# Kernel optimization log

Measured on AMD Instinct MI355X. Metric: run time of the kernel, lower is better.

Reference implementation:

```python
import math
import jax, jax.numpy as jnp
import numpy as np


def _proj(x, w, b):
    # 1x1x1 Conv3d == pointwise channel matmul: (B,C,T,H,W) x (O,C) -> (B,O,T,H,W)
    return jnp.einsum('bcthw,oc->bothw', x, w) + b[None, :, None, None, None]


def setup_inputs() -> dict:
    key = jax.random.key(0)
    ks = jax.random.split(key, 16)
    B, C, T, H, W = 2, 64, 16, 14, 14
    CI = C // 2
    s_in = 1.0 / math.sqrt(C)
    s_out = 1.0 / math.sqrt(CI)
    inp = {'x': jax.random.normal(ks[0], (B, C, T, H, W), jnp.float32)}
    # QKV projections for spatial (s) and temporal (t) branches: (CI, C) weights
    pnames = ['qs', 'ks', 'vs', 'qt', 'kt', 'vt']
    for i, n in enumerate(pnames):
        inp['W' + n] = jax.random.normal(ks[1 + i], (CI, C), jnp.float32) * s_in
        inp['b' + n] = jax.random.normal(ks[7 + i], (CI,), jnp.float32) * 0.01
    # output projection W: (C, CI)
    inp['Ww'] = jax.random.normal(ks[13], (C, CI), jnp.float32) * s_out
    inp['bw'] = jax.random.normal(ks[14], (C,), jnp.float32) * 0.01
    return inp


def reference(x, Wqs, bqs, Wks, bks, Wvs, bvs, Wqt, bqt, Wkt, bkt, Wvt, bvt, Ww, bw):
    B, C, T, H, W = x.shape
    CI = Wqs.shape[0]
    N = CI * H * W  # flat dim after original's raw .view (mixes channel & spatial/time)
    scale = 1.0 / math.sqrt(T)

    # ---- spatial branch: .view(B, T, -1) raw reshape of (B,CI,T,H,W) ----
    qs = _proj(x, Wqs, bqs).reshape(B, T, N).transpose(0, 2, 1)   # (B,N,T)
    ks_ = _proj(x, Wks, bks).reshape(B, T, N)                     # (B,T,N)
    vs = _proj(x, Wvs, bvs).reshape(B, T, N).transpose(0, 2, 1)   # (B,N,T)
    attn_s = jax.nn.softmax(jnp.einsum('bnt,btm->bnm', qs, ks_) * scale, axis=-1)  # (B,N,N)
    ys = jnp.einsum('bnm,bmt->bnt', attn_s, vs)                   # (B,N,T)
    ys = ys.transpose(0, 2, 1).reshape(B, CI, T, H, W)

    # ---- temporal branch: .view(B, CI*H*W, -1) raw reshape ----
    qt = _proj(x, Wqt, bqt).reshape(B, N, T).transpose(0, 2, 1)   # (B,T,N)
    kt = _proj(x, Wkt, bkt).reshape(B, N, T)                      # (B,N,T)
    vt = _proj(x, Wvt, bvt).reshape(B, N, T).transpose(0, 2, 1)   # (B,T,N)
    attn_t = jax.nn.softmax(jnp.einsum('btn,bns->bts', qt, kt) * scale, axis=-1)  # (B,T,T)
    yt = jnp.einsum('bts,bsn->btn', attn_t, vt)                   # (B,T,N)
    yt = yt.transpose(0, 2, 1).reshape(B, CI, T, H, W)

    y = ys + yt
    return _proj(y, Ww, bw) + x
```

## Files before the change

### kernel.cpp

```cpp
#include <hip/hip_runtime.h>
#include <math.h>

#define S3   3136
#define PB   100352
#define XB   200704
#define NN   6272
#define MW   7
#define MPW  896
#define TGC  49

typedef __attribute__((ext_vector_type(8))) short bf16x8;
typedef __attribute__((ext_vector_type(4))) float f32x4;
typedef __attribute__((ext_vector_type(16))) float f32x16;
typedef __attribute__((ext_vector_type(4))) uint u32x4;

__device__ inline ushort f2bf(float f) {
    uint u = __float_as_uint(f);
    return (ushort)((u + 0x7FFFu + ((u >> 16) & 1u)) >> 16);
}

__device__ inline uint cvtpk(float lo, float hi) {
    uint r;
    asm("v_cvt_pk_bf16_f32 %0, %1, %2" : "=v"(r) : "v"(lo), "v"(hi));
    return r;
}

__device__ inline void swap32(uint &a, uint &b) {
    asm("v_permlane32_swap_b32 %0, %1" : "+v"(a), "+v"(b));
}

__global__ __launch_bounds__(256) void proj_kernel(
    const float* __restrict__ x,
    const float* __restrict__ W0, const float* __restrict__ b0,
    const float* __restrict__ W1, const float* __restrict__ b1,
    const float* __restrict__ W2, const float* __restrict__ b2,
    const float* __restrict__ W3, const float* __restrict__ b3,
    const float* __restrict__ W4, const float* __restrict__ b4,
    const float* __restrict__ W5, const float* __restrict__ b5,
    ushort* __restrict__ Qb, ushort* __restrict__ Kb, ushort* __restrict__ Vb,
    float* __restrict__ Qt, float* __restrict__ Kt, float* __restrict__ Vt)
{
    const float* Wp; const float* bp;
    switch (blockIdx.y) {
        case 0:  Wp = W0; bp = b0; break;
        case 1:  Wp = W1; bp = b1; break;
        case 2:  Wp = W2; bp = b2; break;
        case 3:  Wp = W3; bp = b3; break;
        case 4:  Wp = W4; bp = b4; break;
        default: Wp = W5; bp = b5; break;
    }
    int z = blockIdx.z;

    int gid = blockIdx.x * 256 + threadIdx.x;
    if (gid >= 2 * S3) return;
    int b = (gid >= S3) ? 1 : 0;
    int s = gid - b * S3;

    float xr[64];
    #pragma unroll
    for (int c = 0; c < 64; ++c) xr[c] = x[(size_t)b * XB + (size_t)c * S3 + s];

    float a[16];
    #pragma unroll
    for (int oo = 0; oo < 16; ++oo) {
        int o = z * 16 + oo;
        float acc = bp[o];
        #pragma unroll
        for (int c = 0; c < 64; ++c) acc = fmaf(Wp[o * 64 + c], xr[c], acc);
        a[oo] = acc;
    }

    if (blockIdx.y < 2) {
        const float sc = (blockIdx.y == 0) ? 0.36067376022224085f : 1.0f;
        ushort* ob = (blockIdx.y == 0) ? Qb : Kb;
        #pragma unroll
        for (int h = 0; h < 2; ++h) {
            int n = h * S3 + s;
            uint u0 = f2bf(a[0 + h] * sc)  | ((uint)f2bf(a[2 + h]  * sc) << 16);
            uint u1 = f2bf(a[4 + h] * sc)  | ((uint)f2bf(a[6 + h]  * sc) << 16);
            uint u2 = f2bf(a[8 + h] * sc)  | ((uint)f2bf(a[10 + h] * sc) << 16);
            uint u3 = f2bf(a[12 + h] * sc) | ((uint)f2bf(a[14 + h] * sc) << 16);
            *(uint4*)(ob + ((size_t)(b * NN + n) * 16 + z * 8)) = make_uint4(u0, u1, u2, u3);
        }
    } else if (blockIdx.y == 2) {
        #pragma unroll
        for (int oo = 0; oo < 16; ++oo) {
            int o = z * 16 + oo;
            Vb[(size_t)(b * 16 + (o >> 1)) * NN + (o & 1) * S3 + s] = f2bf(a[oo]);
        }
    } else {
        float* op = (blockIdx.y == 3) ? Qt : (blockIdx.y == 4) ? Kt : Vt;
        #pragma unroll
        for (int oo = 0; oo < 16; ++oo)
            op[(size_t)b * PB + (size_t)(z * 16 + oo) * S3 + s] = a[oo];
    }
}

__global__ __launch_bounds__(256) void attn_kernel(
    const ushort* __restrict__ Qb, const ushort* __restrict__ Kb,
    const ushort* __restrict__ Vb, const float* __restrict__ Qt,
    const float* __restrict__ Kt,
    float* __restrict__ Pacc, float* __restrict__ Pl, float* __restrict__ Gp)
{
    __shared__ float qs[128 * 16], ks[128 * 16];

    int b = blockIdx.y;

    if (blockIdx.x >= 343) {
        int c = blockIdx.x - 343;
        size_t base = (size_t)b * PB + (size_t)c * 2048;
        for (int i = threadIdx.x; i < 512; i += 256) {
            ((float4*)qs)[i] = ((const float4*)(Qt + base))[i];
            ((float4*)ks)[i] = ((const float4*)(Kt + base))[i];
        }
        __syncthreads();
        int t = threadIdx.x >> 4, s = threadIdx.x & 15;
        float acc = 0.0f;
        #pragma unroll 8
        for (int n = 0; n < 128; ++n)
            acc = fmaf(qs[n * 16 + t], ks[n * 16 + s], acc);
        Gp[(size_t)(b * TGC + c) * 256 + threadIdx.x] = acc;
        return;
    }

    int wave = __builtin_amdgcn_readfirstlane((int)(threadIdx.x >> 6));
    int lane = threadIdx.x & 63;
    int col  = lane & 31;
    int h    = lane >> 5;
    int gw   = blockIdx.x * 4 + wave;
    int ntile = gw / 7;
    int w     = gw - ntile * 7;
    int nbase = ntile * 32;
    int m0    = w * MPW;

    bf16x8 qf = *(const bf16x8*)(Qb + ((size_t)(b * NN + nbase + col) * 16 + h * 8));

    const bf16x8 vzero = {0, 0, 0, 0, 0, 0, 0, 0};
    const bf16x8 vones = {16256, 16256, 16256, 16256, 16256, 16256, 16256, 16256};
    f32x16 yacc;
    #pragma unroll
    for (int r = 0; r < 16; ++r) yacc[r] = 0.0f;
    f32x16 zero16 = yacc;

    #pragma unroll 2
    for (int it = 0; it < MPW / 32; ++it) {
        int mb = m0 + it * 32;
        bf16x8 kf = *(const bf16x8*)(Kb + ((size_t)(b * NN + mb + col) * 16 + h * 8));
        bf16x8 vf0 = vzero, vf1 = vzero;
        if (col < 16) {
            const ushort* vp = Vb + ((size_t)(b * 16 + col) * NN + mb + h * 8);
            vf0 = *(const bf16x8*)(vp);
            vf1 = *(const bf16x8*)(vp + 16);
        } else if (col == 16) { vf0 = vones; vf1 = vones; }

        f32x16 st = __builtin_amdgcn_mfma_f32_32x32x16_bf16(kf, qf, zero16, 0, 0, 0);
        float pv[16];
        #pragma unroll
        for (int r = 0; r < 16; ++r) pv[r] = __builtin_amdgcn_exp2f(st[r]);

        uint X0 = cvtpk(pv[0],  pv[1]),  X1 = cvtpk(pv[2],  pv[3]);
        uint Y0 = cvtpk(pv[4],  pv[5]),  Y1 = cvtpk(pv[6],  pv[7]);
        uint X2 = cvtpk(pv[8],  pv[9]),  X3 = cvtpk(pv[10], pv[11]);
        uint Y2 = cvtpk(pv[12], pv[13]), Y3 = cvtpk(pv[14], pv[15]);
        swap32(X0, Y0); swap32(X1, Y1);
        swap32(X2, Y2); swap32(X3, Y3);
        u32x4 pb0 = {X0, X1, Y0, Y1};
        u32x4 pb1 = {X2, X3, Y2, Y3};

        yacc = __builtin_amdgcn_mfma_f32_32x32x16_bf16(
                   vf0, __builtin_bit_cast(bf16x8, pb0), yacc, 0, 0, 0);
        yacc = __builtin_amdgcn_mfma_f32_32x32x16_bf16(
                   vf1, __builtin_bit_cast(bf16x8, pb1), yacc, 0, 0, 0);
    }

    #pragma unroll
    for (int r = 0; r < 8; ++r) {
        int t = (r & 3) + 8 * (r >> 2) + 4 * h;
        Pacc[((size_t)(b * 16 + t) * MW + w) * NN + nbase + col] = yacc[r];
    }
    if (h == 0)
        Pl[((size_t)b * MW + w) * NN + nbase + col] = yacc[8];
}

__global__ __launch_bounds__(256) void merge_final(
    const float* __restrict__ Pacc, const float* __restrict__ Pl,
    const float* __restrict__ Gp, const float* __restrict__ Vt,
    const float* __restrict__ x, const float* __restrict__ Ww,
    const float* __restrict__ bw, float* __restrict__ out)
{
    __shared__ float Lsh[256];
    __shared__ float Ash[16][17];
    __shared__ float Wsh[64 * 36];
    __shared__ float Ysh[16 * 36];

    int b  = blockIdx.y;
    int sc = blockIdx.x;

    {
        float a = 0.0f;
        for (int c = 0; c < TGC; ++c)
            a += Gp[(size_t)(b * TGC + c) * 256 + threadIdx.x];
        Lsh[threadIdx.x] = a * 0.25f;
        for (int i = threadIdx.x; i < 2048; i += 256)
            Wsh[(i >> 5) * 36 + (i & 31)] = Ww[i];
    }
    __syncthreads();
    if (threadIdx.x < 16) {
        int t = threadIdx.x;
        const float* Lr = &Lsh[t * 16];
        float mx = -1e30f;
        #pragma unroll
        for (int s = 0; s < 16; ++s) mx = fmaxf(mx, Lr[s]);
        float e[16]; float sm = 0.0f;
        #pragma unroll
        for (int s = 0; s < 16; ++s) { e[s] = __expf(Lr[s] - mx); sm += e[s]; }
        float inv = 1.0f / sm;
        #pragma unroll
        for (int s = 0; s < 16; ++s) Ash[s][t] = e[s] * inv;
    }
    __syncthreads();

    #pragma unroll
    for (int k = 0; k < 2; ++k) {
        int idx = threadIdx.x + k * 256;
        int ss = idx & 15;
        int ci = idx >> 4;
        int s  = sc * 16 + ss;
        int t  = ci >> 1;
        int nn = (ci & 1) * S3 + s;

        float a = 0.0f, l = 0.0f;
        #pragma unroll
        for (int w = 0; w < MW; ++w) {
            a += Pacc[((size_t)(b * 16 + t) * MW + w) * NN + nn];
            l += Pl[((size_t)b * MW + w) * NN + nn];
        }
        float ys = a / l;

        int t2 = nn & 15;
        const float4* vp = (const float4*)(Vt + (size_t)b * PB + (size_t)t * NN + (nn & ~15));
        float4 v0 = vp[0], v1 = vp[1], v2 = vp[2], v3 = vp[3];
        float yt = Ash[0][t2] * v0.x;
        yt = fmaf(Ash[1][t2],  v0.y, yt); yt = fmaf(Ash[2][t2],  v0.z, yt);
        yt = fmaf(Ash[3][t2],  v0.w, yt); yt = fmaf(Ash[4][t2],  v1.x, yt);
        yt = fmaf(Ash[5][t2],  v1.y, yt); yt = fmaf(Ash[6][t2],  v1.z, yt);
        yt = fmaf(Ash[7][t2],  v1.w, yt); yt = fmaf(Ash[8][t2],  v2.x, yt);
        yt = fmaf(Ash[9][t2],  v2.y, yt); yt = fmaf(Ash[10][t2], v2.z, yt);
        yt = fmaf(Ash[11][t2], v2.w, yt); yt = fmaf(Ash[12][t2], v3.x, yt);
        yt = fmaf(Ash[13][t2], v3.y, yt); yt = fmaf(Ash[14][t2], v3.z, yt);
        yt = fmaf(Ash[15][t2], v3.w, yt);

        Ysh[ss * 36 + ci] = ys + yt;
    }
    __syncthreads();

    int ss = threadIdx.x & 15;
    int cg = threadIdx.x >> 4;
    int s  = sc * 16 + ss;

    float acc[4];
    #pragma unroll
    for (int k = 0; k < 4; ++k) acc[k] = bw[cg * 4 + k];

    #pragma unroll
    for (int cb = 0; cb < 32; cb += 4) {
        float4 y4 = *(const float4*)&Ysh[ss * 36 + cb];
        #pragma unroll
        for (int k = 0; k < 4; ++k) {
            float4 w4 = *(const float4*)&Wsh[(cg * 4 + k) * 36 + cb];
            acc[k] = fmaf(w4.x, y4.x, acc[k]);
            acc[k] = fmaf(w4.y, y4.y, acc[k]);
            acc[k] = fmaf(w4.z, y4.z, acc[k]);
            acc[k] = fmaf(w4.w, y4.w, acc[k]);
        }
    }

    #pragma unroll
    for (int k = 0; k < 4; ++k) {
        int c = cg * 4 + k;
        size_t o = (size_t)b * XB + (size_t)c * S3 + s;
        out[o] = x[o] + acc[k];
    }
}

extern "C" void kernel_launch(void* const* d_in, const int* in_sizes, int n_in,
                              void* d_out, int out_size, void* d_ws, size_t ws_size,
                              hipStream_t stream)
{
    const float* x   = (const float*)d_in[0];
    const float* Wqs = (const float*)d_in[1];  const float* bqs = (const float*)d_in[2];
    const float* Wks = (const float*)d_in[3];  const float* bks = (const float*)d_in[4];
    const float* Wvs = (const float*)d_in[5];  const float* bvs = (const float*)d_in[6];
    const float* Wqt = (const float*)d_in[7];  const float* bqt = (const float*)d_in[8];
    const float* Wkt = (const float*)d_in[9];  const float* bkt = (const float*)d_in[10];
    const float* Wvt = (const float*)d_in[11]; const float* bvt = (const float*)d_in[12];
    const float* Ww  = (const float*)d_in[13]; const float* bw  = (const float*)d_in[14];

    float* ws = (float*)d_ws;
    ushort* Qb = (ushort*)(ws);
    ushort* Kb = (ushort*)(ws + 100352);
    ushort* Vb = (ushort*)(ws + 200704);
    float* Qt  = ws + 301056;
    float* Kt  = ws + 501760;
    float* Vt  = ws + 702464;
    float* Gp  = ws + 903168;
    float* Pacc = ws + 928256;
    float* Pl   = ws + 2333184;

    proj_kernel<<<dim3(25, 6, 2), 256, 0, stream>>>(
        x, Wqs, bqs, Wks, bks, Wvs, bvs, Wqt, bqt, Wkt, bkt, Wvt, bvt,
        Qb, Kb, Vb, Qt, Kt, Vt);

    attn_kernel<<<dim3(343 + TGC, 2), 256, 0, stream>>>(
        Qb, Kb, Vb, Qt, Kt, Pacc, Pl, Gp);

    merge_final<<<dim3(196, 2), 256, 0, stream>>>(
        Pacc, Pl, Gp, Vt, x, Ww, bw, (float*)d_out);
}
```

Before: 131.0 us.

## Fuse three kernels into one persistent kernel with software grid barriers

```diff
diff --git a/kernel.cpp b/kernel.cpp
--- a/kernel.cpp
+++ b/kernel.cpp
@@ -10,7 +10,6 @@
 #define TGC  49
 
 typedef __attribute__((ext_vector_type(8))) short bf16x8;
-typedef __attribute__((ext_vector_type(4))) float f32x4;
 typedef __attribute__((ext_vector_type(16))) float f32x16;
 typedef __attribute__((ext_vector_type(4))) uint u32x4;
 
@@ -29,7 +28,27 @@
     asm("v_permlane32_swap_b32 %0, %1" : "+v"(a), "+v"(b));
 }
 
-__global__ __launch_bounds__(256) void proj_kernel(
+__device__ inline void gridbar(uint* bar, int phase) {
+    __syncthreads();
+    if (threadIdx.x == 0) {
+        uint* grp  = bar + phase * 528 + ((blockIdx.x >> 4) << 4);
+        uint* root = bar + phase * 528 + 512;
+        uint old = __hip_atomic_fetch_add(grp, 1u, __ATOMIC_ACQ_REL,
+                                          __HIP_MEMORY_SCOPE_AGENT);
+        if (old == 15u)
+            __hip_atomic_fetch_add(root, 1u, __ATOMIC_ACQ_REL,
+                                   __HIP_MEMORY_SCOPE_AGENT);
+        long spins = 0;
+        while (__hip_atomic_load(root, __ATOMIC_ACQUIRE,
+                                 __HIP_MEMORY_SCOPE_AGENT) < 32u) {
+            __builtin_amdgcn_s_sleep(8);
+            if (++spins > 20000000L) break;
+        }
+    }
+    __syncthreads();
+}
+
+__global__ __launch_bounds__(256, 2) void fused_kernel(
     const float* __restrict__ x,
     const float* __restrict__ W0, const float* __restrict__ b0,
     const float* __restrict__ W1, const float* __restrict__ b1,
@@ -37,249 +56,254 @@
     const float* __restrict__ W3, const float* __restrict__ b3,
     const float* __restrict__ W4, const float* __restrict__ b4,
     const float* __restrict__ W5, const float* __restrict__ b5,
+    const float* __restrict__ Ww, const float* __restrict__ bw,
     ushort* __restrict__ Qb, ushort* __restrict__ Kb, ushort* __restrict__ Vb,
-    float* __restrict__ Qt, float* __restrict__ Kt, float* __restrict__ Vt)
+    float* __restrict__ Qt, float* __restrict__ Kt, float* __restrict__ Vt,
+    float* __restrict__ Gp, float* __restrict__ Pacc, float* __restrict__ Pl,
+    uint* __restrict__ bar, float* __restrict__ out)
 {
-    const float* Wp; const float* bp;
-    switch (blockIdx.y) {
-        case 0:  Wp = W0; bp = b0; break;
-        case 1:  Wp = W1; bp = b1; break;
-        case 2:  Wp = W2; bp = b2; break;
-        case 3:  Wp = W3; bp = b3; break;
-        case 4:  Wp = W4; bp = b4; break;
-        default: Wp = W5; bp = b5; break;
+    __shared__ float shpool[4096];
+    int bid = blockIdx.x;
+    int tid = threadIdx.x;
+
+    if (bid < 300) {
+        int u  = bid;
+        int bx = u % 25;
+        int yq = (u / 25) % 6;
+        int z  = u / 150;
+        const float* Wp; const float* bp;
+        switch (yq) {
+            case 0:  Wp = W0; bp = b0; break;
+            case 1:  Wp = W1; bp = b1; break;
+            case 2:  Wp = W2; bp = b2; break;
+            case 3:  Wp = W3; bp = b3; break;
+            case 4:  Wp = W4; bp = b4; break;
+            default: Wp = W5; bp = b5; break;
+        }
+        int gid = bx * 256 + tid;
+        if (gid < 2 * S3) {
+            int b = (gid >= S3) ? 1 : 0;
+            int s = gid - b * S3;
+
+            float xr[64];
+            #pragma unroll
+            for (int c = 0; c < 64; ++c) xr[c] = x[(size_t)b * XB + (size_t)c * S3 + s];
+
+            float a[16];
+            #pragma unroll
+            for (int oo = 0; oo < 16; ++oo) {
+                int o = z * 16 + oo;
+                float acc = bp[o];
+                #pragma unroll
+                for (int c = 0; c < 64; ++c) acc = fmaf(Wp[o * 64 + c], xr[c], acc);
+                a[oo] = acc;
+            }
+
+            if (yq < 2) {
+                const float sc = (yq == 0) ? 0.36067376022224085f : 1.0f;
+                ushort* ob = (yq == 0) ? Qb : Kb;
+                #pragma unroll
+                for (int h = 0; h < 2; ++h) {
+                    int n = h * S3 + s;
+                    uint u0 = f2bf(a[0 + h] * sc)  | ((uint)f2bf(a[2 + h]  * sc) << 16);
+                    uint u1 = f2bf(a[4 + h] * sc)  | ((uint)f2bf(a[6 + h]  * sc) << 16);
+                    uint u2 = f2bf(a[8 + h] * sc)  | ((uint)f2bf(a[10 + h] * sc) << 16);
+                    uint u3 = f2bf(a[12 + h] * sc) | ((uint)f2bf(a[14 + h] * sc) << 16);
+                    *(uint4*)(ob + ((size_t)(b * NN + n) * 16 + z * 8)) = make_uint4(u0, u1, u2, u3);
+                }
+            } else if (yq == 2) {
+                #pragma unroll
+                for (int oo = 0; oo < 16; ++oo) {
+                    int o = z * 16 + oo;
+                    Vb[(size_t)(b * 16 + (o >> 1)) * NN + (o & 1) * S3 + s] = f2bf(a[oo]);
+                }
+            } else {
+                float* op = (yq == 3) ? Qt : (yq == 4) ? Kt : Vt;
+                #pragma unroll
+                for (int oo = 0; oo < 16; ++oo)
+                    op[(size_t)b * PB + (size_t)(z * 16 + oo) * S3 + s] = a[oo];
+            }
+        }
     }
-    int z = blockIdx.z;
-
-    int gid = blockIdx.x * 256 + threadIdx.x;
-    if (gid >= 2 * S3) return;
-    int b = (gid >= S3) ? 1 : 0;
-    int s = gid - b * S3;
-
-    float xr[64];
-    #pragma unroll
-    for (int c = 0; c < 64; ++c) xr[c] = x[(size_t)b * XB + (size_t)c * S3 + s];
-
-    float a[16];
-    #pragma unroll
-    for (int oo = 0; oo < 16; ++oo) {
-        int o = z * 16 + oo;
-        float acc = bp[o];
+    gridbar(bar, 0);
+
+    for (int u = bid; u < 784; u += 512) {
+        int xb = u % 392;
+        int b  = u / 392;
+
+        if (xb >= 343) {
+            int c = xb - 343;
+            float* qs = shpool;
+            float* ks = shpool + 2048;
+            size_t base = (size_t)b * PB + (size_t)c * 2048;
+            for (int i = tid; i < 512; i += 256) {
+                ((float4*)qs)[i] = ((const float4*)(Qt + base))[i];
+                ((float4*)ks)[i] = ((const float4*)(Kt + base))[i];
+            }
+            __syncthreads();
+            int t = tid >> 4, s = tid & 15;
+            float acc = 0.0f;
+            #pragma unroll 8
+            for (int n = 0; n < 128; ++n)
+                acc = fmaf(qs[n * 16 + t], ks[n * 16 + s], acc);
+            Gp[(size_t)(b * TGC + c) * 256 + tid] = acc;
+            __syncthreads();
+        } else {
+            int wave = __builtin_amdgcn_readfirstlane(tid >> 6);
+            int lane = tid & 63;
+            int col  = lane & 31;
+            int h    = lane >> 5;
+            int gw   = xb * 4 + wave;
+            int ntile = gw / 7;
+            int w     = gw - ntile * 7;
+            int nbase = ntile * 32;
+            int m0    = w * MPW;
+
+            bf16x8 qf = *(const bf16x8*)(Qb + ((size_t)(b * NN + nbase + col) * 16 + h * 8));
+
+            const bf16x8 vzero = {0, 0, 0, 0, 0, 0, 0, 0};
+            const bf16x8 vones = {16256, 16256, 16256, 16256, 16256, 16256, 16256, 16256};
+            f32x16 yacc;
+            #pragma unroll
+            for (int r = 0; r < 16; ++r) yacc[r] = 0.0f;
+            f32x16 zero16 = yacc;
+
+            #pragma unroll 2
+            for (int it = 0; it < MPW / 32; ++it) {
+                int mb = m0 + it * 32;
+                bf16x8 kf = *(const bf16x8*)(Kb + ((size_t)(b * NN + mb + col) * 16 + h * 8));
+                bf16x8 vf0 = vzero, vf1 = vzero;
+                if (col < 16) {
+                    const ushort* vp = Vb + ((size_t)(b * 16 + col) * NN + mb + h * 8);
+                    vf0 = *(const bf16x8*)(vp);
+                    vf1 = *(const bf16x8*)(vp + 16);
+                } else if (col == 16) { vf0 = vones; vf1 = vones; }
+
+                f32x16 st = __builtin_amdgcn_mfma_f32_32x32x16_bf16(kf, qf, zero16, 0, 0, 0);
+                float pv[16];
+                #pragma unroll
+                for (int r = 0; r < 16; ++r) pv[r] = __builtin_amdgcn_exp2f(st[r]);
+
+                uint X0 = cvtpk(pv[0],  pv[1]),  X1 = cvtpk(pv[2],  pv[3]);
+                uint Y0 = cvtpk(pv[4],  pv[5]),  Y1 = cvtpk(pv[6],  pv[7]);
+                uint X2 = cvtpk(pv[8],  pv[9]),  X3 = cvtpk(pv[10], pv[11]);
+                uint Y2 = cvtpk(pv[12], pv[13]), Y3 = cvtpk(pv[14], pv[15]);
+                swap32(X0, Y0); swap32(X1, Y1);
+                swap32(X2, Y2); swap32(X3, Y3);
+                u32x4 pb0 = {X0, X1, Y0, Y1};
+                u32x4 pb1 = {X2, X3, Y2, Y3};
+
+                yacc = __builtin_amdgcn_mfma_f32_32x32x16_bf16(
+                           vf0, __builtin_bit_cast(bf16x8, pb0), yacc, 0, 0, 0);
+                yacc = __builtin_amdgcn_mfma_f32_32x32x16_bf16(
+                           vf1, __builtin_bit_cast(bf16x8, pb1), yacc, 0, 0, 0);
+            }
+
+            #pragma unroll
+            for (int r = 0; r < 8; ++r) {
+                int t = (r & 3) + 8 * (r >> 2) + 4 * h;
+                Pacc[((size_t)(b * 16 + t) * MW + w) * NN + nbase + col] = yacc[r];
+            }
+            if (h == 0)
+                Pl[((size_t)b * MW + w) * NN + nbase + col] = yacc[8];
+        }
+    }
+    gridbar(bar, 1);
+
+    if (bid < 392) {
+        int b  = bid / 196;
+        int sc = bid % 196;
+
+        float* Lsh  = shpool;
+        float* AshF = shpool + 256;
+        float* Wsh  = shpool + 544;
+        float* Ysh  = shpool + 2848;
+
+        {
+            float a = 0.0f;
+            for (int c = 0; c < TGC; ++c)
+                a += Gp[(size_t)(b * TGC + c) * 256 + tid];
+            Lsh[tid] = a * 0.25f;
+            for (int i = tid; i < 2048; i += 256)
+                Wsh[(i >> 5) * 36 + (i & 31)] = Ww[i];
+        }
+        __syncthreads();
+        if (tid < 16) {
+            int t = tid;
+            const float* Lr = &Lsh[t * 16];
+            float mx = -1e30f;
+            #pragma unroll
+            for (int s = 0; s < 16; ++s) mx = fmaxf(mx, Lr[s]);
+            float e[16]; float sm = 0.0f;
+            #pragma unroll
+            for (int s = 0; s < 16; ++s) { e[s] = __expf(Lr[s] - mx); sm += e[s]; }
+            float inv = 1.0f / sm;
+            #pragma unroll
+            for (int s = 0; s < 16; ++s) AshF[s * 17 + t] = e[s] * inv;
+        }
+        __syncthreads();
+
         #pragma unroll
-        for (int c = 0; c < 64; ++c) acc = fmaf(Wp[o * 64 + c], xr[c], acc);
-        a[oo] = acc;
-    }
-
-    if (blockIdx.y < 2) {
-        const float sc = (blockIdx.y == 0) ? 0.36067376022224085f : 1.0f;
-        ushort* ob = (blockIdx.y == 0) ? Qb : Kb;
+        for (int k = 0; k < 2; ++k) {
+            int idx = tid + k * 256;
+            int ss = idx & 15;
+            int ci = idx >> 4;
+            int s  = sc * 16 + ss;
+            int t  = ci >> 1;
+            int nn = (ci & 1) * S3 + s;
+
+            float a = 0.0f, l = 0.0f;
+            #pragma unroll
+            for (int w = 0; w < MW; ++w) {
+                a += Pacc[((size_t)(b * 16 + t) * MW + w) * NN + nn];
+                l += Pl[((size_t)b * MW + w) * NN + nn];
+            }
+            float ys = a / l;
+
+            int t2 = nn & 15;
+            const float4* vp = (const float4*)(Vt + (size_t)b * PB + (size_t)t * NN + (nn & ~15));
+            float4 v0 = vp[0], v1 = vp[1], v2 = vp[2], v3 = vp[3];
+            float yt = AshF[0 * 17 + t2] * v0.x;
+            yt = fmaf(AshF[1 * 17 + t2],  v0.y, yt); yt = fmaf(AshF[2 * 17 + t2],  v0.z, yt);
+            yt = fmaf(AshF[3 * 17 + t2],  v0.w, yt); yt = fmaf(AshF[4 * 17 + t2],  v1.x, yt);
+            yt = fmaf(AshF[5 * 17 + t2],  v1.y, yt); yt = fmaf(AshF[6 * 17 + t2],  v1.z, yt);
+            yt = fmaf(AshF[7 * 17 + t2],  v1.w, yt); yt = fmaf(AshF[8 * 17 + t2],  v2.x, yt);
+            yt = fmaf(AshF[9 * 17 + t2],  v2.y, yt); yt = fmaf(AshF[10 * 17 + t2], v2.z, yt);
+            yt = fmaf(AshF[11 * 17 + t2], v2.w, yt); yt = fmaf(AshF[12 * 17 + t2], v3.x, yt);
+            yt = fmaf(AshF[13 * 17 + t2], v3.y, yt); yt = fmaf(AshF[14 * 17 + t2], v3.z, yt);
+            yt = fmaf(AshF[15 * 17 + t2], v3.w, yt);
+
+            Ysh[ss * 36 + ci] = ys + yt;
+        }
+        __syncthreads();
+
+        int ss = tid & 15;
+        int cg2 = tid >> 4;
+        int s  = sc * 16 + ss;
+
+        float acc[4];
         #pragma unroll
-        for (int h = 0; h < 2; ++h) {
-            int n = h * S3 + s;
-            uint u0 = f2bf(a[0 + h] * sc)  | ((uint)f2bf(a[2 + h]  * sc) << 16);
-            uint u1 = f2bf(a[4 + h] * sc)  | ((uint)f2bf(a[6 + h]  * sc) << 16);
-            uint u2 = f2bf(a[8 + h] * sc)  | ((uint)f2bf(a[10 + h] * sc) << 16);
-            uint u3 = f2bf(a[12 + h] * sc) | ((uint)f2bf(a[14 + h] * sc) << 16);
-            *(uint4*)(ob + ((size_t)(b * NN + n) * 16 + z * 8)) = make_uint4(u0, u1, u2, u3);
-        }
-    } else if (blockIdx.y == 2) {
+        for (int k = 0; k < 4; ++k) acc[k] = bw[cg2 * 4 + k];
+
         #pragma unroll
-        for (int oo = 0; oo < 16; ++oo) {
-            int o = z * 16 + oo;
-            Vb[(size_t)(b * 16 + (o >> 1)) * NN + (o & 1) * S3 + s] = f2bf(a[oo]);
-        }
-    } else {
-        float* op = (blockIdx.y == 3) ? Qt : (blockIdx.y == 4) ? Kt : Vt;
-        #pragma unroll
-        for (int oo = 0; oo < 16; ++oo)
-            op[(size_t)b * PB + (size_t)(z * 16 + oo) * S3 + s] = a[oo];
-    }
-}
-
-__global__ __launch_bounds__(256) void attn_kernel(
-    const ushort* __restrict__ Qb, const ushort* __restrict__ Kb,
-    const ushort* __restrict__ Vb, const float* __restrict__ Qt,
-    const float* __restrict__ Kt,
-    float* __restrict__ Pacc, float* __restrict__ Pl, float* __restrict__ Gp)
-{
-    __shared__ float qs[128 * 16], ks[128 * 16];
-
-    int b = blockIdx.y;
-
-    if (blockIdx.x >= 343) {
-        int c = blockIdx.x - 343;
-        size_t base = (size_t)b * PB + (size_t)c * 2048;
-        for (int i = threadIdx.x; i < 512; i += 256) {
-            ((float4*)qs)[i] = ((const float4*)(Qt + base))[i];
-            ((float4*)ks)[i] = ((const float4*)(Kt + base))[i];
-        }
-        __syncthreads();
-        int t = threadIdx.x >> 4, s = threadIdx.x & 15;
-        float acc = 0.0f;
-        #pragma unroll 8
-        for (int n = 0; n < 128; ++n)
-            acc = fmaf(qs[n * 16 + t], ks[n * 16 + s], acc);
-        Gp[(size_t)(b * TGC + c) * 256 + threadIdx.x] = acc;
-        return;
-    }
-
-    int wave = __builtin_amdgcn_readfirstlane((int)(threadIdx.x >> 6));
-    int lane = threadIdx.x & 63;
-    int col  = lane & 31;
-    int h    = lane >> 5;
-    int gw   = blockIdx.x * 4 + wave;
-    int ntile = gw / 7;
-    int w     = gw - ntile * 7;
-    int nbase = ntile * 32;
-    int m0    = w * MPW;
-
-    bf16x8 qf = *(const bf16x8*)(Qb + ((size_t)(b * NN + nbase + col) * 16 + h * 8));
-
-    const bf16x8 vzero = {0, 0, 0, 0, 0, 0, 0, 0};
-    const bf16x8 vones = {16256, 16256, 16256, 16256, 16256, 16256, 16256, 16256};
-    f32x16 yacc;
-    #pragma unroll
-    for (int r = 0; r < 16; ++r) yacc[r] = 0.0f;
-    f32x16 zero16 = yacc;
-
-    #pragma unroll 2
-    for (int it = 0; it < MPW / 32; ++it) {
-        int mb = m0 + it * 32;
-        bf16x8 kf = *(const bf16x8*)(Kb + ((size_t)(b * NN + mb + col) * 16 + h * 8));
-        bf16x8 vf0 = vzero, vf1 = vzero;
-        if (col < 16) {
-            const ushort* vp = Vb + ((size_t)(b * 16 + col) * NN + mb + h * 8);
-            vf0 = *(const bf16x8*)(vp);
-            vf1 = *(const bf16x8*)(vp + 16);
-        } else if (col == 16) { vf0 = vones; vf1 = vones; }
-
-        f32x16 st = __builtin_amdgcn_mfma_f32_32x32x16_bf16(kf, qf, zero16, 0, 0, 0);
-        float pv[16];
-        #pragma unroll
-        for (int r = 0; r < 16; ++r) pv[r] = __builtin_amdgcn_exp2f(st[r]);
-
-        uint X0 = cvtpk(pv[0],  pv[1]),  X1 = cvtpk(pv[2],  pv[3]);
-        uint Y0 = cvtpk(pv[4],  pv[5]),  Y1 = cvtpk(pv[6],  pv[7]);
-        uint X2 = cvtpk(pv[8],  pv[9]),  X3 = cvtpk(pv[10], pv[11]);
-        uint Y2 = cvtpk(pv[12], pv[13]), Y3 = cvtpk(pv[14], pv[15]);
-        swap32(X0, Y0); swap32(X1, Y1);
-        swap32(X2, Y2); swap32(X3, Y3);
-        u32x4 pb0 = {X0, X1, Y0, Y1};
-        u32x4 pb1 = {X2, X3, Y2, Y3};
-
-        yacc = __builtin_amdgcn_mfma_f32_32x32x16_bf16(
-                   vf0, __builtin_bit_cast(bf16x8, pb0), yacc, 0, 0, 0);
-        yacc = __builtin_amdgcn_mfma_f32_32x32x16_bf16(
-                   vf1, __builtin_bit_cast(bf16x8, pb1), yacc, 0, 0, 0);
-    }
-
-    #pragma unroll
-    for (int r = 0; r < 8; ++r) {
-        int t = (r & 3) + 8 * (r >> 2) + 4 * h;
-        Pacc[((size_t)(b * 16 + t) * MW + w) * NN + nbase + col] = yacc[r];
-    }
-    if (h == 0)
-        Pl[((size_t)b * MW + w) * NN + nbase + col] = yacc[8];
-}
-
-__global__ __launch_bounds__(256) void merge_final(
-    const float* __restrict__ Pacc, const float* __restrict__ Pl,
-    const float* __restrict__ Gp, const float* __restrict__ Vt,
-    const float* __restrict__ x, const float* __restrict__ Ww,
-    const float* __restrict__ bw, float* __restrict__ out)
-{
-    __shared__ float Lsh[256];
-    __shared__ float Ash[16][17];
-    __shared__ float Wsh[64 * 36];
-    __shared__ float Ysh[16 * 36];
-
-    int b  = blockIdx.y;
-    int sc = blockIdx.x;
-
-    {
-        float a = 0.0f;
-        for (int c = 0; c < TGC; ++c)
-            a += Gp[(size_t)(b * TGC + c) * 256 + threadIdx.x];
-        Lsh[threadIdx.x] = a * 0.25f;
-        for (int i = threadIdx.x; i < 2048; i += 256)
-            Wsh[(i >> 5) * 36 + (i & 31)] = Ww[i];
-    }
-    __syncthreads();
-    if (threadIdx.x < 16) {
-        int t = threadIdx.x;
-        const float* Lr = &Lsh[t * 16];
-        float mx = -1e30f;
-        #pragma unroll
-        for (int s = 0; s < 16; ++s) mx = fmaxf(mx, Lr[s]);
-        float e[16]; float sm = 0.0f;
-        #pragma unroll
-        for (int s = 0; s < 16; ++s) { e[s] = __expf(Lr[s] - mx); sm += e[s]; }
-        float inv = 1.0f / sm;
-        #pragma unroll
-        for (int s = 0; s < 16; ++s) Ash[s][t] = e[s] * inv;
-    }
-    __syncthreads();
-
-    #pragma unroll
-    for (int k = 0; k < 2; ++k) {
-        int idx = threadIdx.x + k * 256;
-        int ss = idx & 15;
-        int ci = idx >> 4;
-        int s  = sc * 16 + ss;
-        int t  = ci >> 1;
-        int nn = (ci & 1) * S3 + s;
-
-        float a = 0.0f, l = 0.0f;
-        #pragma unroll
-        for (int w = 0; w < MW; ++w) {
-            a += Pacc[((size_t)(b * 16 + t) * MW + w) * NN + nn];
-            l += Pl[((size_t)b * MW + w) * NN + nn];
-        }
-        float ys = a / l;
-
-        int t2 = nn & 15;
-        const float4* vp = (const float4*)(Vt + (size_t)b * PB + (size_t)t * NN + (nn & ~15));
-        float4 v0 = vp[0], v1 = vp[1], v2 = vp[2], v3 = vp[3];
-        float yt = Ash[0][t2] * v0.x;
-        yt = fmaf(Ash[1][t2],  v0.y, yt); yt = fmaf(Ash[2][t2],  v0.z, yt);
-        yt = fmaf(Ash[3][t2],  v0.w, yt); yt = fmaf(Ash[4][t2],  v1.x, yt);
-        yt = fmaf(Ash[5][t2],  v1.y, yt); yt = fmaf(Ash[6][t2],  v1.z, yt);
-        yt = fmaf(Ash[7][t2],  v1.w, yt); yt = fmaf(Ash[8][t2],  v2.x, yt);
-        yt = fmaf(Ash[9][t2],  v2.y, yt); yt = fmaf(Ash[10][t2], v2.z, yt);
-        yt = fmaf(Ash[11][t2], v2.w, yt); yt = fmaf(Ash[12][t2], v3.x, yt);
-        yt = fmaf(Ash[13][t2], v3.y, yt); yt = fmaf(Ash[14][t2], v3.z, yt);
-        yt = fmaf(Ash[15][t2], v3.w, yt);
-
-        Ysh[ss * 36 + ci] = ys + yt;
-    }
-    __syncthreads();
-
-    int ss = threadIdx.x & 15;
-    int cg = threadIdx.x >> 4;
-    int s  = sc * 16 + ss;
-
-    float acc[4];
-    #pragma unroll
-    for (int k = 0; k < 4; ++k) acc[k] = bw[cg * 4 + k];
-
-    #pragma unroll
-    for (int cb = 0; cb < 32; cb += 4) {
-        float4 y4 = *(const float4*)&Ysh[ss * 36 + cb];
+        for (int cb = 0; cb < 32; cb += 4) {
+            float4 y4 = *(const float4*)&Ysh[ss * 36 + cb];
+            #pragma unroll
+            for (int k = 0; k < 4; ++k) {
+                float4 w4 = *(const float4*)&Wsh[(cg2 * 4 + k) * 36 + cb];
+                acc[k] = fmaf(w4.x, y4.x, acc[k]);
+                acc[k] = fmaf(w4.y, y4.y, acc[k]);
+                acc[k] = fmaf(w4.z, y4.z, acc[k]);
+                acc[k] = fmaf(w4.w, y4.w, acc[k]);
+            }
+        }
+
         #pragma unroll
         for (int k = 0; k < 4; ++k) {
-            float4 w4 = *(const float4*)&Wsh[(cg * 4 + k) * 36 + cb];
-            acc[k] = fmaf(w4.x, y4.x, acc[k]);
-            acc[k] = fmaf(w4.y, y4.y, acc[k]);
-            acc[k] = fmaf(w4.z, y4.z, acc[k]);
-            acc[k] = fmaf(w4.w, y4.w, acc[k]);
-        }
-    }
-
-    #pragma unroll
-    for (int k = 0; k < 4; ++k) {
-        int c = cg * 4 + k;
-        size_t o = (size_t)b * XB + (size_t)c * S3 + s;
-        out[o] = x[o] + acc[k];
+            int c = cg2 * 4 + k;
+            size_t o = (size_t)b * XB + (size_t)c * S3 + s;
+            out[o] = x[o] + acc[k];
+        }
     }
 }
 
@@ -306,14 +330,12 @@
     float* Gp  = ws + 903168;
     float* Pacc = ws + 928256;
     float* Pl   = ws + 2333184;
-
-    proj_kernel<<<dim3(25, 6, 2), 256, 0, stream>>>(
+    uint*  bar  = (uint*)(ws + 2420992);
+    float* out  = (float*)d_out;
+
+    hipMemsetAsync(bar, 0, 2 * 528 * sizeof(uint), stream);
+
+    fused_kernel<<<dim3(512), dim3(256), 0, stream>>>(
         x, Wqs, bqs, Wks, bks, Wvs, bvs, Wqt, bqt, Wkt, bkt, Wvt, bvt,
-        Qb, Kb, Vb, Qt, Kt, Vt);
-
-    attn_kernel<<<dim3(343 + TGC, 2), 256, 0, stream>>>(
-        Qb, Kb, Vb, Qt, Kt, Pacc, Pl, Gp);
-
-    merge_final<<<dim3(196, 2), 256, 0, stream>>>(
-        Pacc, Pl, Gp, Vt, x, Ww, bw, (float*)d_out);
-}
+        Ww, bw, Qb, Kb, Vb, Qt, Kt, Vt, Gp, Pacc, Pl, bar, out);
+}
```

Result: slower. 282.0 us (+115.3%).
